# Optimization experiments

Measured on AMD Instinct MI355X. Metric: run time of the kernel, lower is better.

## Reference

```python
import jax, jax.numpy as jnp
import numpy as np

K = 16
EPS = 1e-5

def _conv1x1(w, b, x):
    # w: [O, I], x: [B, I, N] -> [B, O, N]
    return jnp.einsum('oi,bin->bon', w, x) + b[None, :, None]

def _bn(g, be, m, v, x):
    # inference-mode batchnorm over channel dim of [B, C, N]
    inv = g / jnp.sqrt(v + EPS)
    return x * inv[None, :, None] + (be - m * inv)[None, :, None]

def setup_inputs() -> dict:
    key = jax.random.key(0)
    ks = jax.random.split(key, 16)
    B, C, N = 2, 128, 8192
    d = {}
    d['x'] = jax.random.normal(ks[0], (B, C, N), jnp.float32)
    d['xyz'] = jax.random.normal(ks[1], (B, N, 3), jnp.float32)
    def conv(k, o, i):
        k1, k2 = jax.random.split(k)
        s = 1.0 / np.sqrt(i)
        return (jax.random.uniform(k1, (o, i), jnp.float32, -s, s),
                jax.random.uniform(k2, (o,), jnp.float32, -s, s))
    def bn(k, c):
        return (jax.random.uniform(k, (c,), jnp.float32, 0.5, 1.5),
                jnp.zeros((c,), jnp.float32), jnp.zeros((c,), jnp.float32), jnp.ones((c,), jnp.float32))
    # boundary_net: 2C->C (bn,relu), C->C (bn,relu)
    d['bw1'], d['bb1'] = conv(ks[2], C, 2 * C)
    d['bn1g'], d['bn1b'], d['bn1m'], d['bn1v'] = bn(ks[3], C)
    d['bw2'], d['bb2'] = conv(ks[4], C, C)
    d['bn2g'], d['bn2b'], d['bn2m'], d['bn2v'] = bn(ks[5], C)
    # spatial_relation: 4->32 (bn,relu), 32->64
    d['sw1'], d['sb1'] = conv(ks[6], 32, 4)
    d['sbng'], d['sbnb'], d['sbnm'], d['sbnv'] = bn(ks[7], 32)
    d['sw2'], d['sb2'] = conv(ks[8], 64, 32)
    # attention: C+64 -> C//2 (bn,relu), C//2 -> C, sigmoid
    d['aw1'], d['ab1'] = conv(ks[9], C // 2, C + 64)
    d['abng'], d['abnb'], d['abnm'], d['abnv'] = bn(ks[10], C // 2)
    d['aw2'], d['ab2'] = conv(ks[11], C, C // 2)
    return d

def reference(x, xyz, bw1, bb1, bn1g, bn1b, bn1m, bn1v, bw2, bb2, bn2g, bn2b, bn2m, bn2v,
              sw1, sb1, sbng, sbnb, sbnm, sbnv, sw2, sb2,
              aw1, ab1, abng, abnb, abnm, abnv, aw2, ab2):
    B, C, N = x.shape
    # pairwise squared distances [B, N, N]
    xx = jnp.sum(xyz * xyz, axis=2)  # [B, N]
    dist = xx[:, :, None] + xx[:, None, :] - 2.0 * jnp.einsum('bnd,bmd->bnm', xyz, xyz)
    _, knn_idx = jax.lax.top_k(-dist, K)  # [B, N, K], K smallest distances
    # gather neighbor coords [B, N, K, 3]
    knn_xyz = jax.vmap(lambda p, i: p[i])(xyz, knn_idx)
    rel = knn_xyz - xyz[:, :, None, :]                  # [B, N, K, 3]
    rel_d = jnp.sqrt(jnp.sum(rel * rel, axis=-1))       # [B, N, K]
    mean_rel = jnp.mean(rel, axis=2).transpose(0, 2, 1)   # [B, 3, N]
    mean_d = jnp.mean(rel_d, axis=2)[:, None, :]           # [B, 1, N]
    spatial = jnp.concatenate([mean_rel, mean_d], axis=1)  # [B, 4, N]
    s = jax.nn.relu(_bn(sbng, sbnb, sbnm, sbnv, _conv1x1(sw1, sb1, spatial)))
    spatial_feat = _conv1x1(sw2, sb2, s)  # [B, 64, N]
    # gather neighbor features [B, C, N, K]
    knn_feat = jax.vmap(lambda xb, ib: xb[:, ib])(x, knn_idx)
    max_diff = jnp.max(knn_feat - x[:, :, :, None], axis=3)  # [B, C, N]
    bf = jnp.concatenate([x, max_diff], axis=1)  # [B, 2C, N]
    bf = jax.nn.relu(_bn(bn1g, bn1b, bn1m, bn1v, _conv1x1(bw1, bb1, bf)))
    boundary_feat = jax.nn.relu(_bn(bn2g, bn2b, bn2m, bn2v, _conv1x1(bw2, bb2, bf)))
    ai = jnp.concatenate([x, spatial_feat], axis=1)  # [B, C+64, N]
    a = jax.nn.relu(_bn(abng, abnb, abnm, abnv, _conv1x1(aw1, ab1, ai)))
    attn = jax.nn.sigmoid(_conv1x1(aw2, ab2, a))  # [B, C, N]
    return x + boundary_feat * attn
```

## Files before the change

### kernel.cpp

```cpp
#include <hip/hip_runtime.h>
#include <math.h>

#define NPTS  8192
#define NB    2
#define NTOT  (NPTS*NB)
#define GD    60
#define NCELL (GD*GD*GD)
#define TOTC  (NB*NCELL)
#define HCELL 0.2f
#define INVH  5.0f
#define ORGN  (-6.0f)
#define NN    8192
#define SCAN_CHUNK 1024
#define NBLK_SCAN  ((TOTC + SCAN_CHUNK - 1) / SCAN_CHUNK)
#define RMAX_GRID 4
#define RSTART    2
#define LIST_CAP 512
#define CSEL_CAP 192

#define OFF_CNT     ((size_t)0)
#define OFF_OFFS    (OFF_CNT    + (size_t)TOTC*4)
#define OFF_CELLID  (OFF_OFFS   + (size_t)TOTC*4)
#define OFF_RANK    (OFF_CELLID + (size_t)NTOT*4)
#define OFF_SPOS    (OFF_RANK   + (size_t)NTOT*4)
#define OFF_KNN     (OFF_SPOS   + (size_t)NTOT*16)
#define OFF_SPATIAL (OFF_KNN    + (size_t)NTOT*16*4)
#define OFF_XT      (OFF_SPATIAL+ (size_t)NB*4*NPTS*4)
#define OFF_MD      (OFF_XT     + (size_t)NB*128*NPTS*4)
#define OFF_S1      (OFF_MD     + (size_t)NB*128*NPTS*4)
#define OFF_SF      (OFF_S1     + (size_t)NB*32*NPTS*4)
#define OFF_Y1      (OFF_SF     + (size_t)NB*64*NPTS*4)
#define OFF_Y2      (OFF_Y1     + (size_t)NB*128*NPTS*4)
#define OFF_A1      (OFF_Y2     + (size_t)NB*128*NPTS*4)
#define OFF_SC      (OFF_A1     + (size_t)NB*64*NPTS*4)
#define OFF_BSUM    (OFF_SC     + (size_t)1088*4)
#define OFF_BPRE    (OFF_BSUM   + (size_t)NBLK_SCAN*4)

static __device__ __forceinline__ float sumsq3(float x, float y, float z) {
    return __fadd_rn(__fadd_rn(__fmul_rn(x, x), __fmul_rn(y, y)), __fmul_rn(z, z));
}
static __device__ __forceinline__ float pdist4(float qx, float qy, float qz, float qxx,
                                               float px, float py, float pz) {
    float pxx = sumsq3(px, py, pz);
    float dot = __fadd_rn(__fadd_rn(__fmul_rn(qx, px), __fmul_rn(qy, py)), __fmul_rn(qz, pz));
    return __fsub_rn(__fadd_rn(qxx, pxx), __fadd_rn(dot, dot));
}
static __device__ __forceinline__ unsigned fkey(float f) {
    unsigned b = __float_as_uint(f);
    return b ^ ((unsigned)(((int)b) >> 31) | 0x80000000u);
}
static __device__ __forceinline__ unsigned long long shflx64(unsigned long long v, int m) {
    unsigned lo = __shfl_xor((unsigned)v, m, 64);
    unsigned hi = __shfl_xor((unsigned)(v >> 32), m, 64);
    return ((unsigned long long)hi << 32) | lo;
}
static __device__ __forceinline__ int wave_scan_incl(int v, int lane) {
    #pragma unroll
    for (int d = 1; d < 64; d <<= 1) {
        int u = __shfl_up(v, d, 64);
        v += (lane >= d) ? u : 0;
    }
    return v;
}

__global__ void cell_build(const float* __restrict__ xyz, int* __restrict__ cnt,
                           int* __restrict__ cellid, int* __restrict__ rank) {
    int t = blockIdx.x * 256 + threadIdx.x;
    if (t >= NTOT) return;
    const float* p = xyz + (size_t)t * 3;
    float x = p[0], y = p[1], z = p[2];
    int cx = min(GD - 1, max(0, (int)floorf((x - ORGN) * INVH)));
    int cy = min(GD - 1, max(0, (int)floorf((y - ORGN) * INVH)));
    int cz = min(GD - 1, max(0, (int)floorf((z - ORGN) * INVH)));
    int gcell = (t >> 13) * NCELL + (cz * GD + cy) * GD + cx;
    rank[t] = atomicAdd(&cnt[gcell], 1);
    cellid[t] = gcell;
}

__global__ __launch_bounds__(256) void scan_sums(const int* __restrict__ cnt, int* __restrict__ bsum) {
    __shared__ int red[256];
    int blk = blockIdx.x, t = threadIdx.x;
    int i0 = blk * SCAN_CHUNK + t * 4;
    int s = 0;
    if (i0 + 3 < TOTC) {
        int4 v = *(const int4*)(cnt + i0);
        s = v.x + v.y + v.z + v.w;
    } else {
        for (int j = 0; j < 4; ++j) if (i0 + j < TOTC) s += cnt[i0 + j];
    }
    red[t] = s;
    __syncthreads();
    for (int d = 128; d > 0; d >>= 1) {
        if (t < d) red[t] += red[t + d];
        __syncthreads();
    }
    if (t == 0) bsum[blk] = red[0];
}

__global__ __launch_bounds__(512) void scan_top(const int* __restrict__ bsum, int* __restrict__ bpre) {
    __shared__ int ps[512];
    int t = threadIdx.x;
    int v = (t < NBLK_SCAN) ? bsum[t] : 0;
    ps[t] = v;
    __syncthreads();
    for (int d = 1; d < 512; d <<= 1) {
        int u = 0;
        if (t >= d) u = ps[t - d];
        __syncthreads();
        ps[t] += u;
        __syncthreads();
    }
    if (t < NBLK_SCAN) bpre[t] = ps[t] - v;
}

__global__ __launch_bounds__(256) void scan_write(const int* __restrict__ cnt, const int* __restrict__ bpre,
                                                  int* __restrict__ offs) {
    __shared__ int ps[256];
    int blk = blockIdx.x, t = threadIdx.x;
    int i0 = blk * SCAN_CHUNK + t * 4;
    int a = 0, b = 0, c = 0, d = 0;
    if (i0 + 3 < TOTC) {
        int4 v = *(const int4*)(cnt + i0);
        a = v.x; b = v.y; c = v.z; d = v.w;
    } else {
        if (i0 + 0 < TOTC) a = cnt[i0 + 0];
        if (i0 + 1 < TOTC) b = cnt[i0 + 1];
        if (i0 + 2 < TOTC) c = cnt[i0 + 2];
        if (i0 + 3 < TOTC) d = cnt[i0 + 3];
    }
    int s = a + b + c + d;
    ps[t] = s;
    __syncthreads();
    for (int dd = 1; dd < 256; dd <<= 1) {
        int u = 0;
        if (t >= dd) u = ps[t - dd];
        __syncthreads();
        ps[t] += u;
        __syncthreads();
    }
    int base = bpre[blk] + ps[t] - s;
    if (i0 + 0 < TOTC) offs[i0 + 0] = base;
    if (i0 + 1 < TOTC) offs[i0 + 1] = base + a;
    if (i0 + 2 < TOTC) offs[i0 + 2] = base + a + b;
    if (i0 + 3 < TOTC) offs[i0 + 3] = base + a + b + c;
}

__global__ void scatter_k(const float* __restrict__ xyz, const int* __restrict__ cellid,
                          const int* __restrict__ rank, const int* __restrict__ offs,
                          float4* __restrict__ spos) {
    int t = blockIdx.x * 256 + threadIdx.x;
    if (t >= NTOT) return;
    const float* p = xyz + (size_t)t * 3;
    float x = p[0], y = p[1], z = p[2];
    int pos = offs[cellid[t]] + rank[t];
    spos[pos] = make_float4(x, y, z, __int_as_float(t & (NPTS - 1)));
}

static __device__ __forceinline__ void shell_decode(int R, int u, int& dx, int& dy, int& dz) {
    int L = 2 * R + 1, P = L * L;
    if (u < 2 * P) {
        int v = (u < P) ? u : u - P;
        dz = (u < P) ? -R : R;
        dx = v % L - R;
        dy = v / L - R;
    } else {
        int w = u - 2 * P;
        int ring = w / (8 * R);
        int p = w - ring * 8 * R;
        dz = ring - (R - 1);
        if (p < 2 * R)      { dx = p - R;            dy = -R; }
        else if (p < 4 * R) { dx = R;                dy = p - 3 * R; }
        else if (p < 6 * R) { dx = 5 * R - p;        dy = R; }
        else                { dx = -R;               dy = 7 * R - p; }
    }
}

__global__ __launch_bounds__(64, 4) void knn_kernel(const float4* __restrict__ spos,
                                                    const int* __restrict__ cnt,
                                                    const int* __restrict__ offs,
                                                    int* __restrict__ knn,
                                                    float* __restrict__ spatial) {
    __shared__ unsigned long long buf[16][64];
    __shared__ int lst[LIST_CAP];
    int lane = threadIdx.x;
    int s    = blockIdx.x;
    float4 q = spos[s];
    float qx = q.x, qy = q.y, qz = q.z;
    float qxx = sumsq3(qx, qy, qz);
    int b  = s >> 13;
    int nq = __float_as_int(q.w);
    int cx = min(GD - 1, max(0, (int)floorf((qx - ORGN) * INVH)));
    int cy = min(GD - 1, max(0, (int)floorf((qy - ORGN) * INVH)));
    int cz = min(GD - 1, max(0, (int)floorf((qz - ORGN) * INVH)));
    const int* cb = cnt  + b * NCELL;
    const int* ob = offs + b * NCELL;

    unsigned long long* mybuf = &buf[0][lane];
    unsigned long long minkey = ~0ULL;
    unsigned long long maxkey = 0;
    int nbuf = 0;

    auto process_cells = [&](int num, int base) {
        int rem = num, cur = base;
        while (true) {
            int inc = wave_scan_incl(rem, lane);
            int tot = __shfl(inc, 63, 64);
            if (tot == 0) break;
            int excl = inc - rem;
            int space = LIST_CAP - excl;
            int take = min(rem, max(space, 0));
            for (int j = 0; j < take; ++j) lst[excl + j] = cur + j;
            rem -= take; cur += take;
            int n = min(tot, LIST_CAP);
            asm volatile("s_waitcnt lgkmcnt(0)" ::: "memory");
            __builtin_amdgcn_sched_barrier(0);
            int t = lane;
            int sp_cur = (t < n) ? lst[t] : 0;
            float4 p_cur = spos[sp_cur];
            for (; t < n; t += 64) {
                int tn = t + 64;
                int sp_nx = (tn < n) ? lst[tn] : 0;
                float4 p_nx = spos[sp_nx];
                float d = pdist4(qx, qy, qz, qxx, p_cur.x, p_cur.y, p_cur.z);
                int oi = __float_as_int(p_cur.w);
                unsigned long long key = ((unsigned long long)fkey(d) << 27)
                                       | ((unsigned long long)(unsigned)oi << 14)
                                       | (unsigned)sp_cur;
                if (nbuf < 16) {
                    mybuf[(size_t)nbuf * 64] = key;
                    ++nbuf;
                    minkey = (key < minkey) ? key : minkey;
                    maxkey = (key > maxkey) ? key : maxkey;
                } else if (key < maxkey) {
                    unsigned long long vmax = 0, v2 = 0;
                    int pmax = 0;
                    #pragma unroll
                    for (int j = 0; j < 16; ++j) {
                        unsigned long long v = mybuf[(size_t)j * 64];
                        if (v > vmax) { v2 = vmax; vmax = v; pmax = j; }
                        else if (v > v2) { v2 = v; }
                    }
                    mybuf[(size_t)pmax * 64] = key;
                    maxkey = (key > v2) ? key : v2;
                    minkey = (key < minkey) ? key : minkey;
                }
                sp_cur = sp_nx; p_cur = p_nx;
            }
            asm volatile("s_waitcnt lgkmcnt(0)" ::: "memory");
            __builtin_amdgcn_sched_barrier(0);
        }
    };

    int numA[2] = {0, 0}, baseA[2] = {0, 0};
    #pragma unroll
    for (int h = 0; h < 2; ++h) {
        int u = h * 64 + lane;
        if (u < 125) {
            int dz = u / 25 - 2;
            int rm = u % 25;
            int dy = rm / 5 - 2;
            int dx = rm % 5 - 2;
            int xc = cx + dx, yc = cy + dy, zc = cz + dz;
            if ((unsigned)xc < GD && (unsigned)yc < GD && (unsigned)zc < GD) {
                int cell = (zc * GD + yc) * GD + xc;
                numA[h]  = cb[cell];
                baseA[h] = ob[cell];
            }
        }
    }
    process_cells(numA[0], baseA[0]);
    process_cells(numA[1], baseA[1]);

    float mlx = qx - (ORGN + (float)cx * HCELL);
    float mhx = (ORGN + (float)(cx + 1) * HCELL) - qx;
    float mly = qy - (ORGN + (float)cy * HCELL);
    float mhy = (ORGN + (float)(cy + 1) * HCELL) - qy;
    float mlz = qz - (ORGN + (float)cz * HCELL);
    float mhz = (ORGN + (float)(cz + 1) * HCELL) - qz;
    float margin0 = fminf(fminf(fminf(mlx, mhx), fminf(mly, mhy)), fminf(mlz, mhz));

    int R = RSTART;
    int brute = 0;
    unsigned long long tkey_sel = 0;
    int csel_est = 0;
    while (true) {
        float mR  = margin0 + (float)R * HCELL;
        float mR1 = mR - HCELL;
        float mR2 = mR1 - HCELL;
        unsigned long long tk2 = (mR  > 0.f) ? ((unsigned long long)(fkey(mR  * mR  - 1e-4f) + 1u) << 27) : 0ULL;
        unsigned long long tk1 = (mR1 > 0.f) ? ((unsigned long long)(fkey(mR1 * mR1 - 1e-4f) + 1u) << 27) : 0ULL;
        unsigned long long tk0 = (mR2 > 0.f) ? ((unsigned long long)(fkey(mR2 * mR2 - 1e-4f) + 1u) << 27) : 0ULL;
        unsigned pk01 = 0;
        int c2 = 0;
        for (int j = 0; j < nbuf; ++j) {
            unsigned long long v = mybuf[(size_t)j * 64];
            pk01 += (v < tk0) ? 1u : 0u;
            pk01 += (v < tk1) ? 0x10000u : 0u;
            c2   += (v < tk2) ? 1 : 0;
        }
        for (int o = 32; o > 0; o >>= 1) {
            pk01 += __shfl_xor(pk01, o, 64);
            c2   += __shfl_xor(c2, o, 64);
        }
        if (c2 >= 16) {
            int c0 = (int)(pk01 & 0xFFFFu), c1 = (int)(pk01 >> 16);
            if      (c0 >= 16) { tkey_sel = tk0; csel_est = c0; }
            else if (c1 >= 16) { tkey_sel = tk1; csel_est = c1; }
            else               { tkey_sel = tk2; csel_est = c2; }
            break;
        }
        if (R >= RMAX_GRID) { brute = 1; break; }
        ++R;
        int S = 24 * R * R + 2;
        for (int u0 = 0; u0 < S; u0 += 64) {
            int u = u0 + lane;
            int num = 0, base = 0;
            if (u < S) {
                int dx, dy, dz;
                shell_decode(R, u, dx, dy, dz);
                int xc = cx + dx, yc = cy + dy, zc = cz + dz;
                if ((unsigned)xc < GD && (unsigned)yc < GD && (unsigned)zc < GD) {
                    int cell = (zc * GD + yc) * GD + xc;
                    num  = cb[cell];
                    base = ob[cell];
                }
            }
            process_cells(num, base);
        }
    }

    if (brute) {
        nbuf = 0; minkey = ~0ULL; maxkey = 0;
        int sbase = b << 13;
        for (int i = lane; i < NPTS; i += 64) {
            float4 p = spos[sbase + i];
            float d = pdist4(qx, qy, qz, qxx, p.x, p.y, p.z);
            int oi = __float_as_int(p.w);
            unsigned long long key = ((unsigned long long)fkey(d) << 27)
                                   | ((unsigned long long)(unsigned)oi << 14)
                                   | (unsigned)(sbase + i);
            if (nbuf < 16) {
                mybuf[(size_t)nbuf * 64] = key;
                ++nbuf;
                minkey = (key < minkey) ? key : minkey;
                maxkey = (key > maxkey) ? key : maxkey;
            } else if (key < maxkey) {
                unsigned long long vmax = 0, v2 = 0;
                int pmax = 0;
                #pragma unroll
                for (int j = 0; j < 16; ++j) {
                    unsigned long long v = mybuf[(size_t)j * 64];
                    if (v > vmax) { v2 = vmax; vmax = v; pmax = j; }
                    else if (v > v2) { v2 = v; }
                }
                mybuf[(size_t)pmax * 64] = key;
                maxkey = (key > v2) ? key : v2;
                minkey = (key < minkey) ? key : minkey;
            }
        }
    } else if (csel_est <= CSEL_CAP) {
        int ki = 0;
        for (int j = 0; j < nbuf; ++j) ki += (mybuf[(size_t)j * 64] < tkey_sel) ? 1 : 0;
        int incl = wave_scan_incl(ki, lane);
        int csel = __shfl(incl, 63, 64);
        unsigned long long* sel = (unsigned long long*)&lst[0];
        int w = incl - ki;
        for (int j = 0; j < nbuf; ++j) {
            unsigned long long v = mybuf[(size_t)j * 64];
            if (v < tkey_sel) sel[w++] = v;
        }
        asm volatile("s_waitcnt lgkmcnt(0)" ::: "memory");
        __builtin_amdgcn_sched_barrier(0);
        float rx = 0.f, ry = 0.f, rz = 0.f, rd = 0.f;
        for (int t = lane; t < csel; t += 64) {
            unsigned long long kt = sel[t];
            int r = 0;
            #pragma unroll 4
            for (int j = 0; j < csel; ++j) r += (sel[j] < kt) ? 1 : 0;
            if (r < 16) {
                int sp = (int)(kt & 0x3FFFu);
                int oi = (int)((kt >> 14) & 0x1FFFu);
                float4 p = spos[sp];
                float dx = p.x - qx, dy = p.y - qy, dz = p.z - qz;
                float dl = sqrtf(__fadd_rn(__fadd_rn(__fmul_rn(dx, dx), __fmul_rn(dy, dy)), __fmul_rn(dz, dz)));
                knn[(((size_t)b << 13) + nq) * 16 + r] = oi;
                rx += dx; ry += dy; rz += dz; rd += dl;
            }
        }
        for (int o = 32; o > 0; o >>= 1) {
            rx += __shfl_xor(rx, o, 64);
            ry += __shfl_xor(ry, o, 64);
            rz += __shfl_xor(rz, o, 64);
            rd += __shfl_xor(rd, o, 64);
        }
        if (lane == 0) {
            const float inv16 = 0.0625f;
            spatial[((size_t)b * 4 + 0) * NPTS + nq] = rx * inv16;
            spatial[((size_t)b * 4 + 1) * NPTS + nq] = ry * inv16;
            spatial[((size_t)b * 4 + 2) * NPTS + nq] = rz * inv16;
            spatial[((size_t)b * 4 + 3) * NPTS + nq] = rd * inv16;
        }
        return;
    }

    unsigned long long keep = ~0ULL;
    for (int k = 0; k < 16; ++k) {
        unsigned long long m = minkey;
        for (int o = 32; o > 0; o >>= 1) {
            unsigned long long pv = shflx64(m, o);
            m = (pv < m) ? pv : m;
        }
        unsigned long long bal = __ballot(minkey == m);
        int wl = __ffsll((long long)bal) - 1;
        if (lane == wl) {
            int pos = 0;
            for (int j = 0; j < nbuf; ++j) if (mybuf[(size_t)j * 64] == m) pos = j;
            --nbuf;
            mybuf[(size_t)pos * 64] = mybuf[(size_t)nbuf * 64];
            unsigned long long nm = ~0ULL;
            for (int j = 0; j < nbuf; ++j) {
                unsigned long long v = mybuf[(size_t)j * 64];
                nm = (v < nm) ? v : nm;
            }
            minkey = nm;
        }
        if (lane == k) keep = m;
    }

    float rx = 0.f, ry = 0.f, rz = 0.f, rd = 0.f;
    if (lane < 16) {
        int sp = (int)(keep & 0x3FFFu);
        int oi = (int)((keep >> 14) & 0x1FFFu);
        float4 p = spos[sp];
        rx = p.x - qx; ry = p.y - qy; rz = p.z - qz;
        rd = sqrtf(__fadd_rn(__fadd_rn(__fmul_rn(rx, rx), __fmul_rn(ry, ry)), __fmul_rn(rz, rz)));
        knn[(((size_t)b << 13) + nq) * 16 + lane] = oi;
    }
    for (int o = 8; o > 0; o >>= 1) {
        rx += __shfl_xor(rx, o, 64);
        ry += __shfl_xor(ry, o, 64);
        rz += __shfl_xor(rz, o, 64);
        rd += __shfl_xor(rd, o, 64);
    }
    if (lane == 0) {
        const float inv16 = 0.0625f;
        spatial[((size_t)b * 4 + 0) * NPTS + nq] = rx * inv16;
        spatial[((size_t)b * 4 + 1) * NPTS + nq] = ry * inv16;
        spatial[((size_t)b * 4 + 2) * NPTS + nq] = rz * inv16;
        spatial[((size_t)b * 4 + 3) * NPTS + nq] = rd * inv16;
    }
}

__global__ void transpose_k(const float* __restrict__ x, float* __restrict__ xT) {
    __shared__ float tl[32][33];
    int b = blockIdx.z;
    int n0 = blockIdx.x * 32, c0 = blockIdx.y * 32;
    int tx = threadIdx.x, ty = threadIdx.y;
    const float* xb = x + (size_t)b * 128 * NN;
    float* xtb = xT + (size_t)b * NN * 128;
    for (int i = 0; i < 32; i += 8) tl[ty + i][tx] = xb[(size_t)(c0 + ty + i) * NN + n0 + tx];
    __syncthreads();
    for (int i = 0; i < 32; i += 8) xtb[(size_t)(n0 + ty + i) * 128 + c0 + tx] = tl[tx][ty + i];
}

__global__ __launch_bounds__(256) void md_k(const float* __restrict__ xT,
                                            const int* __restrict__ knn,
                                            float* __restrict__ md) {
    __shared__ int ki[8][16];
    __shared__ float smd[8][132];
    int b = blockIdx.y;
    int n0 = blockIdx.x * 8;
    int tid = threadIdx.x;
    if (tid < 128) ki[tid >> 4][tid & 15] = knn[(((size_t)b << 13) + n0 + (tid >> 4)) * 16 + (tid & 15)];
    __syncthreads();
    int nl = tid >> 5;
    int c4 = (tid & 31) * 4;
    const float* xb = xT + (size_t)b * NPTS * 128;
    float4 m = make_float4(-3.0e38f, -3.0e38f, -3.0e38f, -3.0e38f);
    #pragma unroll
    for (int k = 0; k < 16; ++k) {
        const float4 g = *(const float4*)(xb + (size_t)ki[nl][k] * 128 + c4);
        m.x = fmaxf(m.x, g.x); m.y = fmaxf(m.y, g.y); m.z = fmaxf(m.z, g.z); m.w = fmaxf(m.w, g.w);
    }
    const float4 own = *(const float4*)(xb + (size_t)(n0 + nl) * 128 + c4);
    m.x -= own.x; m.y -= own.y; m.z -= own.z; m.w -= own.w;
    *(float4*)(&smd[nl][c4]) = m;
    __syncthreads();
    for (int r = 0; r < 4; ++r) {
        int c = (tid >> 3) + 32 * r;
        int n2 = tid & 7;
        md[((size_t)b * 128 + c) * NN + n0 + n2] = smd[n2][c];
    }
}

__global__ void prep_k(const float* bb1, const float* g1, const float* be1, const float* m1, const float* v1,
                       const float* bb2, const float* g2, const float* be2, const float* m2, const float* v2,
                       const float* sb1, const float* gs,  const float* bes, const float* ms, const float* vs,
                       const float* sb2,
                       const float* ab1, const float* ga,  const float* bea, const float* ma, const float* va,
                       const float* ab2, float* sc) {
    int t = threadIdx.x;
    if (t < 128) {
        float i1 = g1[t] / sqrtf(v1[t] + 1e-5f);
        sc[t] = i1;        sc[128 + t] = bb1[t] * i1 + be1[t] - m1[t] * i1;
        float i2 = g2[t] / sqrtf(v2[t] + 1e-5f);
        sc[256 + t] = i2;  sc[384 + t] = bb2[t] * i2 + be2[t] - m2[t] * i2;
        sc[832 + t] = 1.0f; sc[960 + t] = ab2[t];
    }
    if (t < 32) {
        float is = gs[t] / sqrtf(vs[t] + 1e-5f);
        sc[512 + t] = is;  sc[544 + t] = sb1[t] * is + bes[t] - ms[t] * is;
    }
    if (t < 64) {
        sc[576 + t] = 1.0f; sc[640 + t] = sb2[t];
        float ia = ga[t] / sqrtf(va[t] + 1e-5f);
        sc[704 + t] = ia;  sc[768 + t] = ab1[t] * ia + bea[t] - ma[t] * ia;
    }
}

template <int O, int K, int TILE_N, int SPLIT, int ACT>
__global__ __launch_bounds__(256) void conv_bn(const float* __restrict__ srcA,
                                               const float* __restrict__ srcB,
                                               const float* __restrict__ W,
                                               const float* __restrict__ scale,
                                               const float* __restrict__ shift,
                                               float* __restrict__ out,
                                               const float* __restrict__ resx,
                                               const float* __restrict__ y2,
                                               float* __restrict__ dout) {
    constexpr int KC  = (K < 64) ? K : 64;
    constexpr int NT4 = TILE_N / 4;
    constexpr int O4  = O / 4;
    static_assert(NT4 * O4 == 256, "thread mapping");
    __shared__ float wT[KC][O + 4];
    __shared__ float inT[KC][TILE_N];
    int tid = threadIdx.x;
    int b = blockIdx.z;
    int n0 = blockIdx.x * TILE_N;
    int n_thr = tid % NT4;
    int o_thr = tid / NT4;
    float acc[4][4] = {{0.f, 0.f, 0.f, 0.f}, {0.f, 0.f, 0.f, 0.f}, {0.f, 0.f, 0.f, 0.f}, {0.f, 0.f, 0.f, 0.f}};

    for (int k0 = 0; k0 < K; k0 += KC) {
        for (int idx = tid; idx < KC * O; idx += 256) {
            int cc = idx % KC;
            int o  = idx / KC;
            wT[cc][o] = W[(size_t)o * K + k0 + cc];
        }
        for (int idx = tid; idx < KC * NT4; idx += 256) {
            int cc = idx / NT4;
            int nf = idx % NT4;
            int cg = k0 + cc;
            const float* src = (cg < SPLIT)
                ? (srcA + ((size_t)b * SPLIT + cg) * NN)
                : (srcB + ((size_t)b * (K - SPLIT) + (cg - SPLIT)) * NN);
            *(float4*)(&inT[cc][nf * 4]) = *(const float4*)(src + n0 + nf * 4);
        }
        __syncthreads();
        #pragma unroll 8
        for (int c = 0; c < KC; ++c) {
            float4 wv = *(const float4*)(&wT[c][o_thr * 4]);
            float4 iv = *(const float4*)(&inT[c][n_thr * 4]);
            acc[0][0] = fmaf(wv.x, iv.x, acc[0][0]); acc[0][1] = fmaf(wv.x, iv.y, acc[0][1]);
            acc[0][2] = fmaf(wv.x, iv.z, acc[0][2]); acc[0][3] = fmaf(wv.x, iv.w, acc[0][3]);
            acc[1][0] = fmaf(wv.y, iv.x, acc[1][0]); acc[1][1] = fmaf(wv.y, iv.y, acc[1][1]);
            acc[1][2] = fmaf(wv.y, iv.z, acc[1][2]); acc[1][3] = fmaf(wv.y, iv.w, acc[1][3]);
            acc[2][0] = fmaf(wv.z, iv.x, acc[2][0]); acc[2][1] = fmaf(wv.z, iv.y, acc[2][1]);
            acc[2][2] = fmaf(wv.z, iv.z, acc[2][2]); acc[2][3] = fmaf(wv.z, iv.w, acc[2][3]);
            acc[3][0] = fmaf(wv.w, iv.x, acc[3][0]); acc[3][1] = fmaf(wv.w, iv.y, acc[3][1]);
            acc[3][2] = fmaf(wv.w, iv.z, acc[3][2]); acc[3][3] = fmaf(wv.w, iv.w, acc[3][3]);
        }
        __syncthreads();
    }
    #pragma unroll
    for (int j = 0; j < 4; ++j) {
        int o = o_thr * 4 + j;
        float scv = scale[o], shv = shift[o];
        float4 v;
        v.x = fmaf(acc[j][0], scv, shv);
        v.y = fmaf(acc[j][1], scv, shv);
        v.z = fmaf(acc[j][2], scv, shv);
        v.w = fmaf(acc[j][3], scv, shv);
        size_t obase = ((size_t)b * O + o) * NN + n0 + n_thr * 4;
        if (ACT == 1) {
            v.x = fmaxf(v.x, 0.f); v.y = fmaxf(v.y, 0.f); v.z = fmaxf(v.z, 0.f); v.w = fmaxf(v.w, 0.f);
            *(float4*)(out + obase) = v;
        } else if (ACT == 2) {
            float4 xr = *(const float4*)(resx + obase);
            float4 yr = *(const float4*)(y2 + obase);
            v.x = xr.x + yr.x / (1.f + __expf(-v.x));
            v.y = xr.y + yr.y / (1.f + __expf(-v.y));
            v.z = xr.z + yr.z / (1.f + __expf(-v.z));
            v.w = xr.w + yr.w / (1.f + __expf(-v.w));
            *(float4*)(dout + obase) = v;
        } else {
            *(float4*)(out + obase) = v;
        }
    }
}

extern "C" void kernel_launch(void* const* d_in, const int* in_sizes, int n_in,
                              void* d_out, int out_size, void* d_ws, size_t ws_size,
                              hipStream_t stream) {
    (void)in_sizes; (void)n_in; (void)out_size; (void)ws_size;
    const float* x    = (const float*)d_in[0];
    const float* xyz  = (const float*)d_in[1];
    const float* bw1  = (const float*)d_in[2];
    const float* bb1  = (const float*)d_in[3];
    const float* bn1g = (const float*)d_in[4];
    const float* bn1b = (const float*)d_in[5];
    const float* bn1m = (const float*)d_in[6];
    const float* bn1v = (const float*)d_in[7];
    const float* bw2  = (const float*)d_in[8];
    const float* bb2  = (const float*)d_in[9];
    const float* bn2g = (const float*)d_in[10];
    const float* bn2b = (const float*)d_in[11];
    const float* bn2m = (const float*)d_in[12];
    const float* bn2v = (const float*)d_in[13];
    const float* sw1  = (const float*)d_in[14];
    const float* sb1  = (const float*)d_in[15];
    const float* sbng = (const float*)d_in[16];
    const float* sbnb = (const float*)d_in[17];
    const float* sbnm = (const float*)d_in[18];
    const float* sbnv = (const float*)d_in[19];
    const float* sw2  = (const float*)d_in[20];
    const float* sb2  = (const float*)d_in[21];
    const float* aw1  = (const float*)d_in[22];
    const float* ab1  = (const float*)d_in[23];
    const float* abng = (const float*)d_in[24];
    const float* abnb = (const float*)d_in[25];
    const float* abnm = (const float*)d_in[26];
    const float* abnv = (const float*)d_in[27];
    const float* aw2  = (const float*)d_in[28];
    const float* ab2  = (const float*)d_in[29];

    char* ws = (char*)d_ws;
    int*    cnt    = (int*)(ws + OFF_CNT);
    int*    offs   = (int*)(ws + OFF_OFFS);
    int*    cellid = (int*)(ws + OFF_CELLID);
    int*    rank   = (int*)(ws + OFF_RANK);
    float4* spos   = (float4*)(ws + OFF_SPOS);
    int*    knn    = (int*)(ws + OFF_KNN);
    float*  spat   = (float*)(ws + OFF_SPATIAL);
    float*  xT     = (float*)(ws + OFF_XT);
    float*  md     = (float*)(ws + OFF_MD);
    float*  s1b    = (float*)(ws + OFF_S1);
    float*  sfb    = (float*)(ws + OFF_SF);
    float*  y1b    = (float*)(ws + OFF_Y1);
    float*  y2b    = (float*)(ws + OFF_Y2);
    float*  a1b    = (float*)(ws + OFF_A1);
    float*  sc     = (float*)(ws + OFF_SC);
    int*    bsum   = (int*)(ws + OFF_BSUM);
    int*    bpre   = (int*)(ws + OFF_BPRE);
    float*  dout   = (float*)d_out;

    hipMemsetAsync(cnt, 0, (size_t)TOTC * 4, stream);
    cell_build<<<dim3((NTOT + 255) / 256), 256, 0, stream>>>(xyz, cnt, cellid, rank);
    scan_sums<<<dim3(NBLK_SCAN), 256, 0, stream>>>(cnt, bsum);
    scan_top<<<dim3(1), 512, 0, stream>>>(bsum, bpre);
    scan_write<<<dim3(NBLK_SCAN), 256, 0, stream>>>(cnt, bpre, offs);
    scatter_k<<<dim3((NTOT + 255) / 256), 256, 0, stream>>>(xyz, cellid, rank, offs, spos);
    knn_kernel<<<dim3(NTOT), 64, 0, stream>>>(spos, cnt, offs, knn, spat);
    transpose_k<<<dim3(NPTS / 32, 128 / 32, NB), dim3(32, 8), 0, stream>>>(x, xT);
    md_k<<<dim3(NPTS / 8, NB), 256, 0, stream>>>(xT, knn, md);
    prep_k<<<1, 128, 0, stream>>>(bb1, bn1g, bn1b, bn1m, bn1v,
                                  bb2, bn2g, bn2b, bn2m, bn2v,
                                  sb1, sbng, sbnb, sbnm, sbnv,
                                  sb2,
                                  ab1, abng, abnb, abnm, abnv,
                                  ab2, sc);
    conv_bn<32, 4, 128, 4, 1><<<dim3(NPTS / 128, 1, NB), 256, 0, stream>>>(
        spat, spat, sw1, sc + 512, sc + 544, s1b, nullptr, nullptr, nullptr);
    conv_bn<64, 32, 64, 32, 0><<<dim3(NPTS / 64, 1, NB), 256, 0, stream>>>(
        s1b, s1b, sw2, sc + 576, sc + 640, sfb, nullptr, nullptr, nullptr);
    conv_bn<128, 256, 32, 128, 1><<<dim3(NPTS / 32, 1, NB), 256, 0, stream>>>(
        x, md, bw1, sc + 0, sc + 128, y1b, nullptr, nullptr, nullptr);
    conv_bn<128, 128, 32, 128, 1><<<dim3(NPTS / 32, 1, NB), 256, 0, stream>>>(
        y1b, y1b, bw2, sc + 256, sc + 384, y2b, nullptr, nullptr, nullptr);
    conv_bn<64, 192, 64, 128, 1><<<dim3(NPTS / 64, 1, NB), 256, 0, stream>>>(
        x, sfb, aw1, sc + 704, sc + 768, a1b, nullptr, nullptr, nullptr);
    conv_bn<128, 64, 32, 64, 2><<<dim3(NPTS / 32, 1, NB), 256, 0, stream>>>(
        a1b, a1b, aw2, sc + 832, sc + 960, dout, x, y2b, dout);
}
```

Before: 395.7 us.

## Rework grid KNN to scan x-row cell ranges and radius-filter candidates

The KNN kernel now reads contiguous per-row cell ranges (a new int2 start/end array written by the scan) instead of per-cell count/offset lookups, so one x-row of cells becomes a single run. Candidates are filtered against a final radius bound and compacted into a shared-memory selection list, replacing the per-lane 16-entry top-k buffer insertion. Shells are expanded by row runs, and the brute-force fallback uses a distance ladder to pick a threshold before ranking. Block indices are also permuted to interleave queries across the batch. The cost is larger shared memory (12 KB per block, and the min-waves launch bound is dropped), which may lower occupancy, plus more complex control flow.

```diff
diff --git a/kernel.cpp b/kernel.cpp
--- a/kernel.cpp
+++ b/kernel.cpp
@@ -15,8 +15,8 @@
 #define NBLK_SCAN  ((TOTC + SCAN_CHUNK - 1) / SCAN_CHUNK)
 #define RMAX_GRID 4
 #define RSTART    2
-#define LIST_CAP 512
-#define CSEL_CAP 192
+#define LIST_CAP 1024
+#define SEL_CAP  1024
 
 #define OFF_CNT     ((size_t)0)
 #define OFF_OFFS    (OFF_CNT    + (size_t)TOTC*4)
@@ -35,6 +35,7 @@
 #define OFF_SC      (OFF_A1     + (size_t)NB*64*NPTS*4)
 #define OFF_BSUM    (OFF_SC     + (size_t)1088*4)
 #define OFF_BPRE    (OFF_BSUM   + (size_t)NBLK_SCAN*4)
+#define OFF_RNG     (((OFF_BPRE + (size_t)NBLK_SCAN*4) + 15) & ~(size_t)15)
 
 static __device__ __forceinline__ float sumsq3(float x, float y, float z) {
     return __fadd_rn(__fadd_rn(__fmul_rn(x, x), __fmul_rn(y, y)), __fmul_rn(z, z));
@@ -114,7 +115,7 @@
 }
 
 __global__ __launch_bounds__(256) void scan_write(const int* __restrict__ cnt, const int* __restrict__ bpre,
-                                                  int* __restrict__ offs) {
+                                                  int* __restrict__ offs, int2* __restrict__ rng) {
     __shared__ int ps[256];
     int blk = blockIdx.x, t = threadIdx.x;
     int i0 = blk * SCAN_CHUNK + t * 4;
@@ -139,10 +140,20 @@
         __syncthreads();
     }
     int base = bpre[blk] + ps[t] - s;
-    if (i0 + 0 < TOTC) offs[i0 + 0] = base;
-    if (i0 + 1 < TOTC) offs[i0 + 1] = base + a;
-    if (i0 + 2 < TOTC) offs[i0 + 2] = base + a + b;
-    if (i0 + 3 < TOTC) offs[i0 + 3] = base + a + b + c;
+    if (i0 + 3 < TOTC) {
+        offs[i0 + 0] = base;
+        offs[i0 + 1] = base + a;
+        offs[i0 + 2] = base + a + b;
+        offs[i0 + 3] = base + a + b + c;
+        *(int4*)(rng + i0)     = make_int4(base, base + a, base + a, base + a + b);
+        *(int4*)(rng + i0 + 2) = make_int4(base + a + b, base + a + b + c,
+                                           base + a + b + c, base + s);
+    } else {
+        if (i0 + 0 < TOTC) { offs[i0 + 0] = base;             rng[i0 + 0] = make_int2(base, base + a); }
+        if (i0 + 1 < TOTC) { offs[i0 + 1] = base + a;         rng[i0 + 1] = make_int2(base + a, base + a + b); }
+        if (i0 + 2 < TOTC) { offs[i0 + 2] = base + a + b;     rng[i0 + 2] = make_int2(base + a + b, base + a + b + c); }
+        if (i0 + 3 < TOTC) { offs[i0 + 3] = base + a + b + c; rng[i0 + 3] = make_int2(base + a + b + c, base + s); }
+    }
 }
 
 __global__ void scatter_k(const float* __restrict__ xyz, const int* __restrict__ cellid,
@@ -156,34 +167,16 @@
     spos[pos] = make_float4(x, y, z, __int_as_float(t & (NPTS - 1)));
 }
 
-static __device__ __forceinline__ void shell_decode(int R, int u, int& dx, int& dy, int& dz) {
-    int L = 2 * R + 1, P = L * L;
-    if (u < 2 * P) {
-        int v = (u < P) ? u : u - P;
-        dz = (u < P) ? -R : R;
-        dx = v % L - R;
-        dy = v / L - R;
-    } else {
-        int w = u - 2 * P;
-        int ring = w / (8 * R);
-        int p = w - ring * 8 * R;
-        dz = ring - (R - 1);
-        if (p < 2 * R)      { dx = p - R;            dy = -R; }
-        else if (p < 4 * R) { dx = R;                dy = p - 3 * R; }
-        else if (p < 6 * R) { dx = 5 * R - p;        dy = R; }
-        else                { dx = -R;               dy = 7 * R - p; }
-    }
-}
-
-__global__ __launch_bounds__(64, 4) void knn_kernel(const float4* __restrict__ spos,
-                                                    const int* __restrict__ cnt,
-                                                    const int* __restrict__ offs,
-                                                    int* __restrict__ knn,
-                                                    float* __restrict__ spatial) {
-    __shared__ unsigned long long buf[16][64];
-    __shared__ int lst[LIST_CAP];
+__global__ __launch_bounds__(64) void knn_kernel(const float4* __restrict__ spos,
+                                                 const int2* __restrict__ rng,
+                                                 int* __restrict__ knn,
+                                                 float* __restrict__ spatial) {
+    __shared__ __align__(16) char shraw[12288];
+    int* lst = (int*)shraw;
+    unsigned long long* sel = (unsigned long long*)(shraw + 4096);
     int lane = threadIdx.x;
-    int s    = blockIdx.x;
+    int bid  = blockIdx.x;
+    int s = (bid & 7) * (NTOT / 8) + (bid >> 3);
     float4 q = spos[s];
     float qx = q.x, qy = q.y, qz = q.z;
     float qxx = sumsq3(qx, qy, qz);
@@ -192,40 +185,188 @@
     int cx = min(GD - 1, max(0, (int)floorf((qx - ORGN) * INVH)));
     int cy = min(GD - 1, max(0, (int)floorf((qy - ORGN) * INVH)));
     int cz = min(GD - 1, max(0, (int)floorf((qz - ORGN) * INVH)));
-    const int* cb = cnt  + b * NCELL;
-    const int* ob = offs + b * NCELL;
-
-    unsigned long long* mybuf = &buf[0][lane];
-    unsigned long long minkey = ~0ULL;
-    unsigned long long maxkey = 0;
-    int nbuf = 0;
-
-    auto process_cells = [&](int num, int base) {
-        int rem = num, cur = base;
-        while (true) {
+    const int2* rg = rng + b * NCELL;
+
+    float mlx = qx - (ORGN + (float)cx * HCELL);
+    float mhx = (ORGN + (float)(cx + 1) * HCELL) - qx;
+    float mly = qy - (ORGN + (float)cy * HCELL);
+    float mhy = (ORGN + (float)(cy + 1) * HCELL) - qy;
+    float mlz = qz - (ORGN + (float)cz * HCELL);
+    float mhz = (ORGN + (float)(cz + 1) * HCELL) - qz;
+    float margin0 = fminf(fminf(fminf(mlx, mhx), fminf(mly, mhy)), fminf(mlz, mhz));
+
+    float mfin = margin0 + (float)(RMAX_GRID + 1) * HCELL;
+    unsigned long long tkfin = (mfin > 0.f)
+        ? ((unsigned long long)(fkey(mfin * mfin - 1e-4f) + 1u) << 27) : 0ULL;
+
+    int tot = 0, ovf = 0;
+
+    auto scan_runs = [&](int num, int start) {
+        int rem = num, cur = start;
+        for (;;) {
             int inc = wave_scan_incl(rem, lane);
-            int tot = __shfl(inc, 63, 64);
-            if (tot == 0) break;
+            int ctot = __shfl(inc, 63, 64);
+            if (ctot == 0) break;
             int excl = inc - rem;
             int space = LIST_CAP - excl;
             int take = min(rem, max(space, 0));
             for (int j = 0; j < take; ++j) lst[excl + j] = cur + j;
             rem -= take; cur += take;
-            int n = min(tot, LIST_CAP);
+            int n = min(ctot, LIST_CAP);
             asm volatile("s_waitcnt lgkmcnt(0)" ::: "memory");
             __builtin_amdgcn_sched_barrier(0);
-            int t = lane;
-            int sp_cur = (t < n) ? lst[t] : 0;
+            int sp_cur = (lane < n) ? lst[lane] : 0;
             float4 p_cur = spos[sp_cur];
-            for (; t < n; t += 64) {
-                int tn = t + 64;
+            for (int t0 = 0; t0 < n; t0 += 64) {
+                int tt = t0 + lane, tn = tt + 64;
                 int sp_nx = (tn < n) ? lst[tn] : 0;
                 float4 p_nx = spos[sp_nx];
-                float d = pdist4(qx, qy, qz, qxx, p_cur.x, p_cur.y, p_cur.z);
-                int oi = __float_as_int(p_cur.w);
+                unsigned long long key = ~0ULL;
+                if (tt < n) {
+                    float d = pdist4(qx, qy, qz, qxx, p_cur.x, p_cur.y, p_cur.z);
+                    key = ((unsigned long long)fkey(d) << 27)
+                        | ((unsigned long long)(unsigned)__float_as_int(p_cur.w) << 14)
+                        | (unsigned)sp_cur;
+                }
+                bool pass = (tt < n) && (key < tkfin);
+                unsigned long long mk = __ballot(pass);
+                int cnum = (int)__popcll(mk);
+                if (tot + cnum > SEL_CAP) { ovf = 1; return; }
+                if (pass) sel[tot + (int)__popcll(mk & ((1ULL << lane) - 1ULL))] = key;
+                tot += cnum;
+                sp_cur = sp_nx; p_cur = p_nx;
+            }
+            asm volatile("s_waitcnt lgkmcnt(0)" ::: "memory");
+            __builtin_amdgcn_sched_barrier(0);
+        }
+    };
+
+    int brute = (tkfin == 0ULL) ? 1 : 0;
+
+    if (!brute) {
+        int Lb = 2 * RSTART + 1;
+        int nrows = Lb * Lb;
+        int num = 0, start = 0;
+        if (lane < nrows) {
+            int dzr = lane / Lb - RSTART, dyr = lane % Lb - RSTART;
+            int zc = cz + dzr, yc = cy + dyr;
+            if ((unsigned)zc < GD && (unsigned)yc < GD) {
+                int rowb = (zc * GD + yc) * GD;
+                int xlo = max(cx - RSTART, 0), xhi = min(cx + RSTART, GD - 1);
+                start = rg[rowb + xlo].x;
+                num   = rg[rowb + xhi].y - start;
+            }
+        }
+        scan_runs(num, start);
+        if (ovf) brute = 1;
+    }
+
+    int R = RSTART;
+    unsigned long long tkey_sel = ~0ULL;
+    int cselq = 0;
+    while (!brute) {
+        float mR  = margin0 + (float)R * HCELL;
+        float mR1 = mR - HCELL, mR2 = mR1 - HCELL;
+        unsigned long long tk2 = (mR  > 0.f) ? ((unsigned long long)(fkey(mR  * mR  - 1e-4f) + 1u) << 27) : 0ULL;
+        unsigned long long tk1 = (mR1 > 0.f) ? ((unsigned long long)(fkey(mR1 * mR1 - 1e-4f) + 1u) << 27) : 0ULL;
+        unsigned long long tk0 = (mR2 > 0.f) ? ((unsigned long long)(fkey(mR2 * mR2 - 1e-4f) + 1u) << 27) : 0ULL;
+        unsigned pk01 = 0; int c2 = 0;
+        for (int t0 = 0; t0 < tot; t0 += 64) {
+            int tt = t0 + lane;
+            if (tt < tot) {
+                unsigned long long v = sel[tt];
+                pk01 += (v < tk0) ? 1u : 0u;
+                pk01 += (v < tk1) ? 0x10000u : 0u;
+                c2   += (v < tk2) ? 1 : 0;
+            }
+        }
+        for (int o = 32; o > 0; o >>= 1) { pk01 += __shfl_xor(pk01, o, 64); c2 += __shfl_xor(c2, o, 64); }
+        if (c2 >= 16) {
+            int c0 = (int)(pk01 & 0xFFFFu), c1 = (int)(pk01 >> 16);
+            if      (c0 >= 16) { tkey_sel = tk0; cselq = c0; }
+            else if (c1 >= 16) { tkey_sel = tk1; cselq = c1; }
+            else               { tkey_sel = tk2; cselq = c2; }
+            break;
+        }
+        if (R >= RMAX_GRID) { brute = 1; break; }
+        ++R;
+        int Ls = 2 * R + 1;
+        int P = Ls * Ls, P2 = (Ls - 2) * (Ls - 2);
+        int nruns = P + P2;
+        for (int r0 = 0; r0 < nruns && !ovf; r0 += 64) {
+            int u = r0 + lane;
+            int num = 0, start = 0;
+            if (u < nruns) {
+                int dzr, dyr, xlo, xhi;
+                if (u < P) {
+                    dzr = u / Ls - R; dyr = u % Ls - R;
+                    bool outer = (dzr == -R || dzr == R || dyr == -R || dyr == R);
+                    if (outer) { xlo = max(cx - R, 0); xhi = min(cx + R, GD - 1); }
+                    else       { xlo = cx - R; xhi = cx - R; }
+                } else {
+                    int v = u - P; int L2 = Ls - 2;
+                    dzr = v / L2 - (R - 1); dyr = v % L2 - (R - 1);
+                    xlo = cx + R; xhi = cx + R;
+                }
+                int zc = cz + dzr, yc = cy + dyr;
+                if ((unsigned)zc < GD && (unsigned)yc < GD && xlo >= 0 && xhi < GD) {
+                    int rowb = (zc * GD + yc) * GD;
+                    start = rg[rowb + xlo].x;
+                    num   = rg[rowb + xhi].y - start;
+                }
+            }
+            scan_runs(num, start);
+        }
+        if (ovf) brute = 1;
+    }
+
+    if (brute) {
+        const float LADR[16] = {0.35f, 0.4725f, 0.637875f, 0.86113125f,
+                                1.1625272f, 1.5694117f, 2.1187058f, 2.8602529f,
+                                3.8613414f, 5.2128109f, 7.0372947f, 9.5003478f,
+                                12.825470f, 17.314384f, 23.374418f, 31.555464f};
+        int sbase = b << 13;
+        int cc[16];
+        #pragma unroll
+        for (int k = 0; k < 16; ++k) cc[k] = 0;
+        for (int i0 = 0; i0 < NPTS; i0 += 64) {
+            float4 p = spos[sbase + i0 + lane];
+            float d = pdist4(qx, qy, qz, qxx, p.x, p.y, p.z);
+            #pragma unroll
+            for (int k = 0; k < 16; ++k) cc[k] += (d < LADR[k] * LADR[k]) ? 1 : 0;
+        }
+        #pragma unroll
+        for (int k = 0; k < 16; ++k)
+            for (int o = 32; o > 0; o >>= 1) cc[k] += __shfl_xor(cc[k], o, 64);
+        float Tq = LADR[15] * LADR[15]; int cL = cc[15];
+        #pragma unroll
+        for (int k = 14; k >= 0; --k) if (cc[k] >= 16) { Tq = LADR[k] * LADR[k]; cL = cc[k]; }
+        if (cL <= SEL_CAP) {
+            tot = 0;
+            for (int i0 = 0; i0 < NPTS; i0 += 64) {
+                int idx = sbase + i0 + lane;
+                float4 p = spos[idx];
+                float d = pdist4(qx, qy, qz, qxx, p.x, p.y, p.z);
+                bool pass = (d < Tq);
                 unsigned long long key = ((unsigned long long)fkey(d) << 27)
-                                       | ((unsigned long long)(unsigned)oi << 14)
-                                       | (unsigned)sp_cur;
+                                       | ((unsigned long long)(unsigned)__float_as_int(p.w) << 14)
+                                       | (unsigned)idx;
+                unsigned long long mk = __ballot(pass);
+                if (pass) sel[tot + (int)__popcll(mk & ((1ULL << lane) - 1ULL))] = key;
+                tot += (int)__popcll(mk);
+            }
+            tkey_sel = ~0ULL;
+            cselq = tot;
+        } else {
+            unsigned long long* mybuf = ((unsigned long long*)shraw) + lane;
+            unsigned long long minkey = ~0ULL, maxkey = 0;
+            int nbuf = 0;
+            for (int i = lane; i < NPTS; i += 64) {
+                float4 p = spos[sbase + i];
+                float d = pdist4(qx, qy, qz, qxx, p.x, p.y, p.z);
+                unsigned long long key = ((unsigned long long)fkey(d) << 27)
+                                       | ((unsigned long long)(unsigned)__float_as_int(p.w) << 14)
+                                       | (unsigned)(sbase + i);
                 if (nbuf < 16) {
                     mybuf[(size_t)nbuf * 64] = key;
                     ++nbuf;
@@ -244,210 +385,109 @@
                     maxkey = (key > v2) ? key : v2;
                     minkey = (key < minkey) ? key : minkey;
                 }
-                sp_cur = sp_nx; p_cur = p_nx;
-            }
-            asm volatile("s_waitcnt lgkmcnt(0)" ::: "memory");
-            __builtin_amdgcn_sched_barrier(0);
-        }
-    };
-
-    int numA[2] = {0, 0}, baseA[2] = {0, 0};
-    #pragma unroll
-    for (int h = 0; h < 2; ++h) {
-        int u = h * 64 + lane;
-        if (u < 125) {
-            int dz = u / 25 - 2;
-            int rm = u % 25;
-            int dy = rm / 5 - 2;
-            int dx = rm % 5 - 2;
-            int xc = cx + dx, yc = cy + dy, zc = cz + dz;
-            if ((unsigned)xc < GD && (unsigned)yc < GD && (unsigned)zc < GD) {
-                int cell = (zc * GD + yc) * GD + xc;
-                numA[h]  = cb[cell];
-                baseA[h] = ob[cell];
-            }
-        }
-    }
-    process_cells(numA[0], baseA[0]);
-    process_cells(numA[1], baseA[1]);
-
-    float mlx = qx - (ORGN + (float)cx * HCELL);
-    float mhx = (ORGN + (float)(cx + 1) * HCELL) - qx;
-    float mly = qy - (ORGN + (float)cy * HCELL);
-    float mhy = (ORGN + (float)(cy + 1) * HCELL) - qy;
-    float mlz = qz - (ORGN + (float)cz * HCELL);
-    float mhz = (ORGN + (float)(cz + 1) * HCELL) - qz;
-    float margin0 = fminf(fminf(fminf(mlx, mhx), fminf(mly, mhy)), fminf(mlz, mhz));
-
-    int R = RSTART;
-    int brute = 0;
-    unsigned long long tkey_sel = 0;
-    int csel_est = 0;
-    while (true) {
-        float mR  = margin0 + (float)R * HCELL;
-        float mR1 = mR - HCELL;
-        float mR2 = mR1 - HCELL;
-        unsigned long long tk2 = (mR  > 0.f) ? ((unsigned long long)(fkey(mR  * mR  - 1e-4f) + 1u) << 27) : 0ULL;
-        unsigned long long tk1 = (mR1 > 0.f) ? ((unsigned long long)(fkey(mR1 * mR1 - 1e-4f) + 1u) << 27) : 0ULL;
-        unsigned long long tk0 = (mR2 > 0.f) ? ((unsigned long long)(fkey(mR2 * mR2 - 1e-4f) + 1u) << 27) : 0ULL;
-        unsigned pk01 = 0;
-        int c2 = 0;
-        for (int j = 0; j < nbuf; ++j) {
-            unsigned long long v = mybuf[(size_t)j * 64];
-            pk01 += (v < tk0) ? 1u : 0u;
-            pk01 += (v < tk1) ? 0x10000u : 0u;
-            c2   += (v < tk2) ? 1 : 0;
-        }
-        for (int o = 32; o > 0; o >>= 1) {
-            pk01 += __shfl_xor(pk01, o, 64);
-            c2   += __shfl_xor(c2, o, 64);
-        }
-        if (c2 >= 16) {
-            int c0 = (int)(pk01 & 0xFFFFu), c1 = (int)(pk01 >> 16);
-            if      (c0 >= 16) { tkey_sel = tk0; csel_est = c0; }
-            else if (c1 >= 16) { tkey_sel = tk1; csel_est = c1; }
-            else               { tkey_sel = tk2; csel_est = c2; }
-            break;
-        }
-        if (R >= RMAX_GRID) { brute = 1; break; }
-        ++R;
-        int S = 24 * R * R + 2;
-        for (int u0 = 0; u0 < S; u0 += 64) {
-            int u = u0 + lane;
-            int num = 0, base = 0;
-            if (u < S) {
-                int dx, dy, dz;
-                shell_decode(R, u, dx, dy, dz);
-                int xc = cx + dx, yc = cy + dy, zc = cz + dz;
-                if ((unsigned)xc < GD && (unsigned)yc < GD && (unsigned)zc < GD) {
-                    int cell = (zc * GD + yc) * GD + xc;
-                    num  = cb[cell];
-                    base = ob[cell];
+            }
+            unsigned long long keep = ~0ULL;
+            for (int k = 0; k < 16; ++k) {
+                unsigned long long m = minkey;
+                for (int o = 32; o > 0; o >>= 1) {
+                    unsigned long long pv = shflx64(m, o);
+                    m = (pv < m) ? pv : m;
                 }
-            }
-            process_cells(num, base);
-        }
-    }
-
-    if (brute) {
-        nbuf = 0; minkey = ~0ULL; maxkey = 0;
-        int sbase = b << 13;
-        for (int i = lane; i < NPTS; i += 64) {
-            float4 p = spos[sbase + i];
-            float d = pdist4(qx, qy, qz, qxx, p.x, p.y, p.z);
-            int oi = __float_as_int(p.w);
-            unsigned long long key = ((unsigned long long)fkey(d) << 27)
-                                   | ((unsigned long long)(unsigned)oi << 14)
-                                   | (unsigned)(sbase + i);
-            if (nbuf < 16) {
-                mybuf[(size_t)nbuf * 64] = key;
-                ++nbuf;
-                minkey = (key < minkey) ? key : minkey;
-                maxkey = (key > maxkey) ? key : maxkey;
-            } else if (key < maxkey) {
-                unsigned long long vmax = 0, v2 = 0;
-                int pmax = 0;
-                #pragma unroll
-                for (int j = 0; j < 16; ++j) {
-                    unsigned long long v = mybuf[(size_t)j * 64];
-                    if (v > vmax) { v2 = vmax; vmax = v; pmax = j; }
-                    else if (v > v2) { v2 = v; }
+                unsigned long long bal = __ballot(minkey == m);
+                int wl = __ffsll((long long)bal) - 1;
+                if (lane == wl) {
+                    int pos = 0;
+                    for (int j = 0; j < nbuf; ++j) if (mybuf[(size_t)j * 64] == m) pos = j;
+                    --nbuf;
+                    mybuf[(size_t)pos * 64] = mybuf[(size_t)nbuf * 64];
+                    unsigned long long nm = ~0ULL;
+                    for (int j = 0; j < nbuf; ++j) {
+                        unsigned long long v = mybuf[(size_t)j * 64];
+                        nm = (v < nm) ? v : nm;
+                    }
+                    minkey = nm;
                 }
-                mybuf[(size_t)pmax * 64] = key;
-                maxkey = (key > v2) ? key : v2;
-                minkey = (key < minkey) ? key : minkey;
-            }
-        }
-    } else if (csel_est <= CSEL_CAP) {
-        int ki = 0;
-        for (int j = 0; j < nbuf; ++j) ki += (mybuf[(size_t)j * 64] < tkey_sel) ? 1 : 0;
-        int incl = wave_scan_incl(ki, lane);
-        int csel = __shfl(incl, 63, 64);
-        unsigned long long* sel = (unsigned long long*)&lst[0];
-        int w = incl - ki;
-        for (int j = 0; j < nbuf; ++j) {
-            unsigned long long v = mybuf[(size_t)j * 64];
-            if (v < tkey_sel) sel[w++] = v;
+                if (lane == k) keep = m;
+            }
+            float rx = 0.f, ry = 0.f, rz = 0.f, rd = 0.f;
+            if (lane < 16) {
+                int sp = (int)(keep & 0x3FFFu);
+                int oi = (int)((keep >> 14) & 0x1FFFu);
+                float4 p = spos[sp];
+                rx = p.x - qx; ry = p.y - qy; rz = p.z - qz;
+                rd = sqrtf(__fadd_rn(__fadd_rn(__fmul_rn(rx, rx), __fmul_rn(ry, ry)), __fmul_rn(rz, rz)));
+                knn[(((size_t)b << 13) + nq) * 16 + lane] = oi;
+            }
+            for (int o = 8; o > 0; o >>= 1) {
+                rx += __shfl_xor(rx, o, 64);
+                ry += __shfl_xor(ry, o, 64);
+                rz += __shfl_xor(rz, o, 64);
+                rd += __shfl_xor(rd, o, 64);
+            }
+            if (lane == 0) {
+                const float inv16 = 0.0625f;
+                spatial[((size_t)b * 4 + 0) * NPTS + nq] = rx * inv16;
+                spatial[((size_t)b * 4 + 1) * NPTS + nq] = ry * inv16;
+                spatial[((size_t)b * 4 + 2) * NPTS + nq] = rz * inv16;
+                spatial[((size_t)b * 4 + 3) * NPTS + nq] = rd * inv16;
+            }
+            return;
+        }
+    }
+
+    asm volatile("s_waitcnt lgkmcnt(0)" ::: "memory");
+    __builtin_amdgcn_sched_barrier(0);
+    unsigned long long* sel2 = (unsigned long long*)shraw;
+    const unsigned long long* src;
+    int m;
+    if (cselq <= 512) {
+        int w = 0;
+        for (int t0 = 0; t0 < tot; t0 += 64) {
+            int tt = t0 + lane;
+            unsigned long long v = (tt < tot) ? sel[tt] : ~0ULL;
+            bool pass = (tt < tot) && (v < tkey_sel);
+            unsigned long long mk = __ballot(pass);
+            if (pass) sel2[w + (int)__popcll(mk & ((1ULL << lane) - 1ULL))] = v;
+            w += (int)__popcll(mk);
         }
         asm volatile("s_waitcnt lgkmcnt(0)" ::: "memory");
         __builtin_amdgcn_sched_barrier(0);
-        float rx = 0.f, ry = 0.f, rz = 0.f, rd = 0.f;
-        for (int t = lane; t < csel; t += 64) {
-            unsigned long long kt = sel[t];
-            int r = 0;
-            #pragma unroll 4
-            for (int j = 0; j < csel; ++j) r += (sel[j] < kt) ? 1 : 0;
-            if (r < 16) {
-                int sp = (int)(kt & 0x3FFFu);
-                int oi = (int)((kt >> 14) & 0x1FFFu);
-                float4 p = spos[sp];
-                float dx = p.x - qx, dy = p.y - qy, dz = p.z - qz;
-                float dl = sqrtf(__fadd_rn(__fadd_rn(__fmul_rn(dx, dx), __fmul_rn(dy, dy)), __fmul_rn(dz, dz)));
-                knn[(((size_t)b << 13) + nq) * 16 + r] = oi;
-                rx += dx; ry += dy; rz += dz; rd += dl;
-            }
-        }
-        for (int o = 32; o > 0; o >>= 1) {
-            rx += __shfl_xor(rx, o, 64);
-            ry += __shfl_xor(ry, o, 64);
-            rz += __shfl_xor(rz, o, 64);
-            rd += __shfl_xor(rd, o, 64);
-        }
-        if (lane == 0) {
-            const float inv16 = 0.0625f;
-            spatial[((size_t)b * 4 + 0) * NPTS + nq] = rx * inv16;
-            spatial[((size_t)b * 4 + 1) * NPTS + nq] = ry * inv16;
-            spatial[((size_t)b * 4 + 2) * NPTS + nq] = rz * inv16;
-            spatial[((size_t)b * 4 + 3) * NPTS + nq] = rd * inv16;
-        }
-        return;
-    }
-
-    unsigned long long keep = ~0ULL;
-    for (int k = 0; k < 16; ++k) {
-        unsigned long long m = minkey;
-        for (int o = 32; o > 0; o >>= 1) {
-            unsigned long long pv = shflx64(m, o);
-            m = (pv < m) ? pv : m;
-        }
-        unsigned long long bal = __ballot(minkey == m);
-        int wl = __ffsll((long long)bal) - 1;
-        if (lane == wl) {
-            int pos = 0;
-            for (int j = 0; j < nbuf; ++j) if (mybuf[(size_t)j * 64] == m) pos = j;
-            --nbuf;
-            mybuf[(size_t)pos * 64] = mybuf[(size_t)nbuf * 64];
-            unsigned long long nm = ~0ULL;
-            for (int j = 0; j < nbuf; ++j) {
-                unsigned long long v = mybuf[(size_t)j * 64];
-                nm = (v < nm) ? v : nm;
-            }
-            minkey = nm;
-        }
-        if (lane == k) keep = m;
-    }
-
-    float rx = 0.f, ry = 0.f, rz = 0.f, rd = 0.f;
-    if (lane < 16) {
-        int sp = (int)(keep & 0x3FFFu);
-        int oi = (int)((keep >> 14) & 0x1FFFu);
-        float4 p = spos[sp];
-        rx = p.x - qx; ry = p.y - qy; rz = p.z - qz;
-        rd = sqrtf(__fadd_rn(__fadd_rn(__fmul_rn(rx, rx), __fmul_rn(ry, ry)), __fmul_rn(rz, rz)));
-        knn[(((size_t)b << 13) + nq) * 16 + lane] = oi;
-    }
-    for (int o = 8; o > 0; o >>= 1) {
-        rx += __shfl_xor(rx, o, 64);
-        ry += __shfl_xor(ry, o, 64);
-        rz += __shfl_xor(rz, o, 64);
-        rd += __shfl_xor(rd, o, 64);
+        src = sel2; m = w;
+    } else {
+        src = sel; m = tot;
+    }
+    float rxs = 0.f, rys = 0.f, rzs = 0.f, rds = 0.f;
+    for (int t0 = 0; t0 < m; t0 += 64) {
+        int tt = t0 + lane;
+        if (tt < m) {
+            unsigned long long kt = src[tt];
+            if (kt < tkey_sel) {
+                int rr = 0;
+                for (int j = 0; j < m; ++j) rr += (src[j] < kt) ? 1 : 0;
+                if (rr < 16) {
+                    int sp = (int)(kt & 0x3FFFu);
+                    int oi = (int)((kt >> 14) & 0x1FFFu);
+                    float4 p = spos[sp];
+                    float dx = p.x - qx, dy = p.y - qy, dz = p.z - qz;
+                    float dl = sqrtf(__fadd_rn(__fadd_rn(__fmul_rn(dx, dx), __fmul_rn(dy, dy)), __fmul_rn(dz, dz)));
+                    knn[(((size_t)b << 13) + nq) * 16 + rr] = oi;
+                    rxs += dx; rys += dy; rzs += dz; rds += dl;
+                }
+            }
+        }
+    }
+    for (int o = 32; o > 0; o >>= 1) {
+        rxs += __shfl_xor(rxs, o, 64);
+        rys += __shfl_xor(rys, o, 64);
+        rzs += __shfl_xor(rzs, o, 64);
+        rds += __shfl_xor(rds, o, 64);
     }
     if (lane == 0) {
         const float inv16 = 0.0625f;
-        spatial[((size_t)b * 4 + 0) * NPTS + nq] = rx * inv16;
-        spatial[((size_t)b * 4 + 1) * NPTS + nq] = ry * inv16;
-        spatial[((size_t)b * 4 + 2) * NPTS + nq] = rz * inv16;
-        spatial[((size_t)b * 4 + 3) * NPTS + nq] = rd * inv16;
+        spatial[((size_t)b * 4 + 0) * NPTS + nq] = rxs * inv16;
+        spatial[((size_t)b * 4 + 1) * NPTS + nq] = rys * inv16;
+        spatial[((size_t)b * 4 + 2) * NPTS + nq] = rzs * inv16;
+        spatial[((size_t)b * 4 + 3) * NPTS + nq] = rds * inv16;
     }
 }
 
@@ -652,15 +692,16 @@
     float*  sc     = (float*)(ws + OFF_SC);
     int*    bsum   = (int*)(ws + OFF_BSUM);
     int*    bpre   = (int*)(ws + OFF_BPRE);
+    int2*   rng    = (int2*)(ws + OFF_RNG);
     float*  dout   = (float*)d_out;
 
     hipMemsetAsync(cnt, 0, (size_t)TOTC * 4, stream);
     cell_build<<<dim3((NTOT + 255) / 256), 256, 0, stream>>>(xyz, cnt, cellid, rank);
     scan_sums<<<dim3(NBLK_SCAN), 256, 0, stream>>>(cnt, bsum);
     scan_top<<<dim3(1), 512, 0, stream>>>(bsum, bpre);
-    scan_write<<<dim3(NBLK_SCAN), 256, 0, stream>>>(cnt, bpre, offs);
+    scan_write<<<dim3(NBLK_SCAN), 256, 0, stream>>>(cnt, bpre, offs, rng);
     scatter_k<<<dim3((NTOT + 255) / 256), 256, 0, stream>>>(xyz, cellid, rank, offs, spos);
-    knn_kernel<<<dim3(NTOT), 64, 0, stream>>>(spos, cnt, offs, knn, spat);
+    knn_kernel<<<dim3(NTOT), 64, 0, stream>>>(spos, rng, knn, spat);
     transpose_k<<<dim3(NPTS / 32, 128 / 32, NB), dim3(32, 8), 0, stream>>>(x, xT);
     md_k<<<dim3(NPTS / 8, NB), 256, 0, stream>>>(xT, knn, md);
     prep_k<<<1, 128, 0, stream>>>(bb1, bn1g, bn1b, bn1m, bn1v,
```

Result: faster. 336.2 us (-15.0%).
